# Performance work log

Measured on AMD Instinct MI355X. Metric: run time of the kernel, lower is better.

The kernel has to match this reference:

```python
import jax, jax.numpy as jnp
import numpy as np

TEMPERATURE = 0.07
EPS = 1e-8          # torch cosine_similarity norm clamp
DIAG_FILL = 9e-15   # value masked_fill'ed onto the diagonal BEFORE temperature scaling


def setup_inputs() -> dict:
    key = jax.random.key(0)
    N, D = 16384, 128
    feats = jax.random.normal(key, (N, D), dtype=jnp.float32)
    # unique labels: required for the original torch code's broadcast
    # (-cos_sim[pos_mask] must have exactly N elements)
    labels = jnp.arange(N, dtype=jnp.int32).reshape(N, 1)
    return {"feats": feats, "labels": labels}


def reference(feats, labels):
    # cosine similarity matrix: normalize rows once, then a single GEMM
    norm = jnp.maximum(jnp.linalg.norm(feats, axis=-1, keepdims=True), EPS)
    f = feats / norm
    cos_sim = f @ f.T                                   # [N, N]

    N = cos_sim.shape[0]
    eye = jnp.eye(N, dtype=bool)
    cos_sim = jnp.where(eye, DIAG_FILL, cos_sim)        # masked_fill_(self_mask, 9e-15)
    cos_sim = cos_sim / TEMPERATURE

    pos_mask = labels == labels.T                       # [N, N] bool, one True per row
    # cos_sim[pos_mask] with exactly one positive per row == masked row-sum
    pos = jnp.sum(jnp.where(pos_mask, cos_sim, 0.0), axis=-1)  # [N]

    nll = -pos + jax.nn.logsumexp(cos_sim, axis=-1)     # [N]
    return jnp.mean(nll)
```

## Files before the change

kernel.cpp:

```cpp
#include <hip/hip_runtime.h>
#include <hip/hip_bf16.h>
#include <stdint.h>

typedef __attribute__((ext_vector_type(8))) short short8;
typedef __attribute__((ext_vector_type(4))) float f32x4;

#define N_ROWS 16384
#define DIM 128

constexpr float ALPHA = 4.5398160f;
constexpr float POSC = 1.2857143e-13f;

__device__ __forceinline__ void gload_lds16(const void* g, void* lds) {
  __builtin_amdgcn_global_load_lds(
      (const __attribute__((address_space(1))) void*)(uintptr_t)g,
      (__attribute__((address_space(3))) void*)(uintptr_t)lds,
      16, 0, 0);
}

__global__ void normalize_kernel(const float* __restrict__ feats,
                                 unsigned short* __restrict__ G,
                                 float* __restrict__ rowsum) {
  const int tid  = threadIdx.x;
  const int lane = tid & 63;
  const int row  = blockIdx.x * 4 + (tid >> 6);

  const float2 v = *(const float2*)(feats + (size_t)row * DIM + lane * 2);
  float ss = v.x * v.x + v.y * v.y;
#pragma unroll
  for (int m = 1; m < 64; m <<= 1) ss += __shfl_xor(ss, m);
  const float sc = ALPHA / fmaxf(sqrtf(ss), 1e-8f);

  __hip_bfloat16 h0 = __float2bfloat16(v.x * sc);
  __hip_bfloat16 h1 = __float2bfloat16(v.y * sc);
  unsigned int packed = (unsigned int)(*(unsigned short*)&h0) |
                        ((unsigned int)(*(unsigned short*)&h1) << 16);
  *(unsigned int*)(G + (size_t)row * DIM + lane * 2) = packed;

  if (blockIdx.x < 64) rowsum[blockIdx.x * 256 + tid] = 0.f;
}

__global__ __launch_bounds__(256, 2) void simclr_lse_kernel(
    const unsigned short* __restrict__ G, float* __restrict__ rowsum) {
  const int tid  = threadIdx.x;
  const int lane = tid & 63;
  const int w    = tid >> 6;
  const int wr   = w >> 1;
  const int wc   = w & 1;
  const int c    = lane & 15;
  const int q    = lane >> 4;

  const int p  = blockIdx.x >> 3;
  const int s  = blockIdx.x & 7;
  const int r8 = p & 7;
  const int jb = (s * 129 + r8) >> 3;
  const int je = ((s + 1) * 129 + r8) >> 3;
  const int split = 128 - p;

  __shared__ __align__(16) unsigned short Bbuf[2][128 * 128];

  unsigned goff[8];
#pragma unroll
  for (int t = 0; t < 8; ++t) {
    const int cidx = t * 256 + tid;
    const int col  = cidx >> 4;
    const int kc   = (cidx & 15) ^ (col & 15);
    goff[t] = (unsigned)(col * DIM + kc * 8);
  }

  unsigned boff[4][4];
#pragma unroll
  for (int tc = 0; tc < 4; ++tc)
#pragma unroll
    for (int ks = 0; ks < 4; ++ks) {
      const int col = wc * 64 + tc * 16 + c;
      const int kc  = ks * 4 + q;
      boff[tc][ks] = (unsigned)((col * 16 + (kc ^ c)) * 16);
    }

  const f32x4 zero4 = {0.f, 0.f, 0.f, 0.f};
  const short* Gs = (const short*)G;

  for (int sg = 0; sg < 2; ++sg) {
    int rt, cbeg, nct;
    if (sg == 0) {
      rt   = p;
      cbeg = p + jb;
      nct  = min(je, split) - jb;
    } else {
      rt   = 127 - p;
      const int t0 = max(jb, split);
      cbeg = t0 - 1;
      nct  = je - t0;
    }
    if (nct <= 0) continue;

    const int rbw = rt * 128 + wr * 64;

    short8 afrag[4][4];
#pragma unroll
    for (int tr = 0; tr < 4; ++tr)
#pragma unroll
      for (int ks = 0; ks < 4; ++ks) {
        const int row = rbw + tr * 16 + c;
        afrag[tr][ks] = *(const short8*)(Gs + (size_t)row * DIM + ks * 32 + q * 8);
      }

    float rs[4][4];
#pragma unroll
    for (int tr = 0; tr < 4; ++tr)
#pragma unroll
      for (int r = 0; r < 4; ++r) rs[tr][r] = 0.f;

    {
      const unsigned short* gsrc = G + (size_t)cbeg * 128 * DIM;
#pragma unroll
      for (int t = 0; t < 8; ++t)
        gload_lds16(gsrc + goff[t],
                    (void*)(&Bbuf[0][0] + (size_t)(t * 256 + w * 64) * 8));
    }

    for (int jj = 0; jj < nct; ++jj) {
      const int cur = jj & 1;
      const int ct  = cbeg + jj;
      __syncthreads();

      if (jj + 1 < nct) {
        const unsigned short* gsrc = G + (size_t)(ct + 1) * 128 * DIM;
#pragma unroll
        for (int t = 0; t < 8; ++t)
          gload_lds16(gsrc + goff[t],
                      (void*)(&Bbuf[cur ^ 1][0] + (size_t)(t * 256 + w * 64) * 8));
      }

      const char* bbase = (const char*)&Bbuf[cur][0];
      f32x4 acc[4][4];
#pragma unroll
      for (int ks = 0; ks < 4; ++ks) {
        short8 bfr[4];
#pragma unroll
        for (int tc = 0; tc < 4; ++tc)
          bfr[tc] = *(const short8*)(bbase + boff[tc][ks]);
#pragma unroll
        for (int tr = 0; tr < 4; ++tr)
#pragma unroll
          for (int tc = 0; tc < 4; ++tc) {
            if (ks == 0)
              acc[tr][tc] = __builtin_amdgcn_mfma_f32_16x16x32_bf16(
                  afrag[tr][0], bfr[tc], zero4, 0, 0, 0);
            else
              acc[tr][tc] = __builtin_amdgcn_mfma_f32_16x16x32_bf16(
                  afrag[tr][ks], bfr[tc], acc[tr][tc], 0, 0, 0);
          }
      }

      if (ct == rt && wr == wc) {
#pragma unroll
        for (int tr = 0; tr < 4; ++tr)
#pragma unroll
          for (int r = 0; r < 4; ++r)
            if (c == q * 4 + r) acc[tr][tr][r] = 0.f;
      }

      float cs[4] = {0.f, 0.f, 0.f, 0.f};
#pragma unroll
      for (int tr = 0; tr < 4; ++tr)
#pragma unroll
        for (int tc = 0; tc < 4; ++tc) {
          const float e0 = __builtin_amdgcn_exp2f(acc[tr][tc][0]);
          const float e1 = __builtin_amdgcn_exp2f(acc[tr][tc][1]);
          const float e2 = __builtin_amdgcn_exp2f(acc[tr][tc][2]);
          const float e3 = __builtin_amdgcn_exp2f(acc[tr][tc][3]);
          rs[tr][0] += e0;
          rs[tr][1] += e1;
          rs[tr][2] += e2;
          rs[tr][3] += e3;
          cs[tc] += (e0 + e1) + (e2 + e3);
        }

      if (ct != rt) {
#pragma unroll
        for (int tc = 0; tc < 4; ++tc) {
          float v = cs[tc];
          v += __shfl_xor(v, 16);
          v += __shfl_xor(v, 32);
          if (q == 0)
            atomicAdd(&rowsum[ct * 128 + wc * 64 + tc * 16 + c], v);
        }
      }
    }

#pragma unroll
    for (int tr = 0; tr < 4; ++tr)
#pragma unroll
      for (int r = 0; r < 4; ++r) {
        float v = rs[tr][r];
        v += __shfl_xor(v, 1);
        v += __shfl_xor(v, 2);
        v += __shfl_xor(v, 4);
        v += __shfl_xor(v, 8);
        if (c == 0) atomicAdd(&rowsum[rbw + tr * 16 + q * 4 + r], v);
      }
    __syncthreads();
  }
}

__global__ void finalize_kernel(const float* __restrict__ rowsum,
                                float* __restrict__ out) {
  const int tid = threadIdx.x;
  float local = 0.f;
  for (int i = tid; i < N_ROWS; i += 1024) local += logf(rowsum[i]);
#pragma unroll
  for (int m = 1; m < 64; m <<= 1) local += __shfl_xor(local, m);
  __shared__ float part[16];
  if ((tid & 63) == 0) part[tid >> 6] = local;
  __syncthreads();
  if (tid == 0) {
    float s = 0.f;
#pragma unroll
    for (int i = 0; i < 16; ++i) s += part[i];
    out[0] = s / (float)N_ROWS - POSC;
  }
}

extern "C" void kernel_launch(void* const* d_in, const int* in_sizes, int n_in,
                              void* d_out, int out_size, void* d_ws, size_t ws_size,
                              hipStream_t stream) {
  (void)in_sizes; (void)n_in; (void)out_size; (void)ws_size;
  const float* feats = (const float*)d_in[0];
  unsigned short* G = (unsigned short*)d_ws;
  float* rowsum = (float*)((char*)d_ws + (size_t)N_ROWS * DIM * 2);

  normalize_kernel<<<dim3(N_ROWS / 4), dim3(256), 0, stream>>>(feats, G, rowsum);
  simclr_lse_kernel<<<dim3(512), dim3(256), 0, stream>>>(G, rowsum);
  finalize_kernel<<<dim3(1), dim3(1024), 0, stream>>>(rowsum, d_out ? (float*)d_out : nullptr);
}
```

Before: 116.6 us.

## Replace column atomics with scratch partials and single-buffer LDS tile

Column-sum atomics on mirrored tiles are replaced by plain stores into a per-tile-pair scratch array, and a new column-reduce kernel sums them into rowsum. The LDS double buffer shrinks to one tile buffer loaded synchronously each iteration, which drops the prefetch overlap but halves shared memory, likely to raise occupancy. Column partials are also skipped on diagonal tiles. The cost is an extra kernel launch and a scratch buffer, and global-load latency is now exposed inside the loop.

```diff
diff --git a/kernel.cpp b/kernel.cpp
--- a/kernel.cpp
+++ b/kernel.cpp
@@ -41,7 +41,8 @@
 }
 
 __global__ __launch_bounds__(256, 2) void simclr_lse_kernel(
-    const unsigned short* __restrict__ G, float* __restrict__ rowsum) {
+    const unsigned short* __restrict__ G, float* __restrict__ rowsum,
+    float* __restrict__ scratchC) {
   const int tid  = threadIdx.x;
   const int lane = tid & 63;
   const int w    = tid >> 6;
@@ -57,7 +58,7 @@
   const int je = ((s + 1) * 129 + r8) >> 3;
   const int split = 128 - p;
 
-  __shared__ __align__(16) unsigned short Bbuf[2][128 * 128];
+  __shared__ __align__(16) unsigned short Tbuf[128 * 128];
 
   unsigned goff[8];
 #pragma unroll
@@ -112,35 +113,25 @@
 #pragma unroll
       for (int r = 0; r < 4; ++r) rs[tr][r] = 0.f;
 
-    {
-      const unsigned short* gsrc = G + (size_t)cbeg * 128 * DIM;
-#pragma unroll
-      for (int t = 0; t < 8; ++t)
-        gload_lds16(gsrc + goff[t],
-                    (void*)(&Bbuf[0][0] + (size_t)(t * 256 + w * 64) * 8));
-    }
-
     for (int jj = 0; jj < nct; ++jj) {
-      const int cur = jj & 1;
-      const int ct  = cbeg + jj;
+      const int ct = cbeg + jj;
       __syncthreads();
-
-      if (jj + 1 < nct) {
-        const unsigned short* gsrc = G + (size_t)(ct + 1) * 128 * DIM;
+      {
+        const unsigned short* gsrc = G + (size_t)ct * 128 * DIM;
 #pragma unroll
         for (int t = 0; t < 8; ++t)
           gload_lds16(gsrc + goff[t],
-                      (void*)(&Bbuf[cur ^ 1][0] + (size_t)(t * 256 + w * 64) * 8));
-      }
-
-      const char* bbase = (const char*)&Bbuf[cur][0];
+                      (void*)(Tbuf + (size_t)(t * 256 + w * 64) * 8));
+      }
+      __syncthreads();
+
       f32x4 acc[4][4];
 #pragma unroll
       for (int ks = 0; ks < 4; ++ks) {
         short8 bfr[4];
 #pragma unroll
         for (int tc = 0; tc < 4; ++tc)
-          bfr[tc] = *(const short8*)(bbase + boff[tc][ks]);
+          bfr[tc] = *(const short8*)((const char*)Tbuf + boff[tc][ks]);
 #pragma unroll
         for (int tr = 0; tr < 4; ++tr)
 #pragma unroll
@@ -162,6 +153,7 @@
             if (c == q * 4 + r) acc[tr][tr][r] = 0.f;
       }
 
+      const bool mirror = (ct != rt);
       float cs[4] = {0.f, 0.f, 0.f, 0.f};
 #pragma unroll
       for (int tr = 0; tr < 4; ++tr)
@@ -175,17 +167,17 @@
           rs[tr][1] += e1;
           rs[tr][2] += e2;
           rs[tr][3] += e3;
-          cs[tc] += (e0 + e1) + (e2 + e3);
+          if (mirror) cs[tc] += (e0 + e1) + (e2 + e3);
         }
 
-      if (ct != rt) {
+      if (mirror) {
+        float* slot = scratchC + (size_t)(ct * (ct - 1) / 2 + rt) * 256 + wr * 128;
 #pragma unroll
         for (int tc = 0; tc < 4; ++tc) {
           float v = cs[tc];
           v += __shfl_xor(v, 16);
           v += __shfl_xor(v, 32);
-          if (q == 0)
-            atomicAdd(&rowsum[ct * 128 + wc * 64 + tc * 16 + c], v);
+          if (q == 0) slot[wc * 64 + tc * 16 + c] = v;
         }
       }
     }
@@ -201,8 +193,21 @@
         v += __shfl_xor(v, 8);
         if (c == 0) atomicAdd(&rowsum[rbw + tr * 16 + q * 4 + r], v);
       }
-    __syncthreads();
   }
+}
+
+__global__ void colreduce_kernel(const float* __restrict__ scratchC,
+                                 float* __restrict__ rowsum) {
+  const int ct  = blockIdx.x;
+  const int j   = threadIdx.x & 127;
+  const int h   = threadIdx.x >> 7;
+  __shared__ float tmp[128];
+  float v = 0.f;
+  const float* base = scratchC + (size_t)(ct * (ct - 1) / 2) * 256 + h * 128 + j;
+  for (int rt = 0; rt < ct; ++rt) v += base[(size_t)rt * 256];
+  if (h == 1) tmp[j] = v;
+  __syncthreads();
+  if (h == 0) rowsum[ct * 128 + j] += v + tmp[j];
 }
 
 __global__ void finalize_kernel(const float* __restrict__ rowsum,
@@ -230,8 +235,10 @@
   const float* feats = (const float*)d_in[0];
   unsigned short* G = (unsigned short*)d_ws;
   float* rowsum = (float*)((char*)d_ws + (size_t)N_ROWS * DIM * 2);
+  float* scratchC = rowsum + N_ROWS;
 
   normalize_kernel<<<dim3(N_ROWS / 4), dim3(256), 0, stream>>>(feats, G, rowsum);
-  simclr_lse_kernel<<<dim3(512), dim3(256), 0, stream>>>(G, rowsum);
+  simclr_lse_kernel<<<dim3(512), dim3(256), 0, stream>>>(G, rowsum, scratchC);
+  colreduce_kernel<<<dim3(128), dim3(256), 0, stream>>>(scratchC, rowsum);
   finalize_kernel<<<dim3(1), dim3(1024), 0, stream>>>(rowsum, d_out ? (float*)d_out : nullptr);
 }
```

After: 155.6 us. 33.5% more time.

## Split MFMA tile into two halves, raise wave priority, branchless diagonal mask

Applied to the files above, without the earlier changes.

Splits the per-tile MFMA accumulation into two column halves, loading B fragments just in time. The GEMM section is wrapped in s_setprio so waves in their matrix phase get issue priority over waves doing exp2 work. The diagonal masking becomes a branchless FMA select on the exponentials, and the trailing __syncthreads between the two row segments is dropped. The intent is better overlap of MFMA and transcendental work across the two waves per SIMD, and fewer live accumulators. Removing the barrier risks an LDS race when the second segment's prefetch overwrites a buffer still being read.

```diff
diff --git a/kernel.cpp b/kernel.cpp
--- a/kernel.cpp
+++ b/kernel.cpp
@@ -77,6 +77,10 @@
       const int kc  = ks * 4 + q;
       boff[tc][ks] = (unsigned)((col * 16 + (kc ^ c)) * 16);
     }
+
+  float dsel[4];
+#pragma unroll
+  for (int r = 0; r < 4; ++r) dsel[r] = (c == q * 4 + r) ? 1.f : 0.f;
 
   const f32x4 zero4 = {0.f, 0.f, 0.f, 0.f};
   const short* Gs = (const short*)G;
@@ -134,51 +138,83 @@
       }
 
       const char* bbase = (const char*)&Bbuf[cur][0];
-      f32x4 acc[4][4];
+
+      __builtin_amdgcn_s_setprio(1);
+      f32x4 acc1[4][2];
 #pragma unroll
       for (int ks = 0; ks < 4; ++ks) {
-        short8 bfr[4];
-#pragma unroll
-        for (int tc = 0; tc < 4; ++tc)
-          bfr[tc] = *(const short8*)(bbase + boff[tc][ks]);
-#pragma unroll
-        for (int tr = 0; tr < 4; ++tr)
-#pragma unroll
-          for (int tc = 0; tc < 4; ++tc) {
-            if (ks == 0)
-              acc[tr][tc] = __builtin_amdgcn_mfma_f32_16x16x32_bf16(
-                  afrag[tr][0], bfr[tc], zero4, 0, 0, 0);
-            else
-              acc[tr][tc] = __builtin_amdgcn_mfma_f32_16x16x32_bf16(
-                  afrag[tr][ks], bfr[tc], acc[tr][tc], 0, 0, 0);
-          }
-      }
-
-      if (ct == rt && wr == wc) {
-#pragma unroll
-        for (int tr = 0; tr < 4; ++tr)
-#pragma unroll
-          for (int r = 0; r < 4; ++r)
-            if (c == q * 4 + r) acc[tr][tr][r] = 0.f;
-      }
-
+        const short8 b0 = *(const short8*)(bbase + boff[0][ks]);
+        const short8 b1 = *(const short8*)(bbase + boff[1][ks]);
+#pragma unroll
+        for (int tr = 0; tr < 4; ++tr) {
+          if (ks == 0) {
+            acc1[tr][0] = __builtin_amdgcn_mfma_f32_16x16x32_bf16(
+                afrag[tr][0], b0, zero4, 0, 0, 0);
+            acc1[tr][1] = __builtin_amdgcn_mfma_f32_16x16x32_bf16(
+                afrag[tr][0], b1, zero4, 0, 0, 0);
+          } else {
+            acc1[tr][0] = __builtin_amdgcn_mfma_f32_16x16x32_bf16(
+                afrag[tr][ks], b0, acc1[tr][0], 0, 0, 0);
+            acc1[tr][1] = __builtin_amdgcn_mfma_f32_16x16x32_bf16(
+                afrag[tr][ks], b1, acc1[tr][1], 0, 0, 0);
+          }
+        }
+      }
+      f32x4 acc2[4][2];
+#pragma unroll
+      for (int ks = 0; ks < 4; ++ks) {
+        const short8 b2 = *(const short8*)(bbase + boff[2][ks]);
+        const short8 b3 = *(const short8*)(bbase + boff[3][ks]);
+#pragma unroll
+        for (int tr = 0; tr < 4; ++tr) {
+          if (ks == 0) {
+            acc2[tr][0] = __builtin_amdgcn_mfma_f32_16x16x32_bf16(
+                afrag[tr][0], b2, zero4, 0, 0, 0);
+            acc2[tr][1] = __builtin_amdgcn_mfma_f32_16x16x32_bf16(
+                afrag[tr][0], b3, zero4, 0, 0, 0);
+          } else {
+            acc2[tr][0] = __builtin_amdgcn_mfma_f32_16x16x32_bf16(
+                afrag[tr][ks], b2, acc2[tr][0], 0, 0, 0);
+            acc2[tr][1] = __builtin_amdgcn_mfma_f32_16x16x32_bf16(
+                afrag[tr][ks], b3, acc2[tr][1], 0, 0, 0);
+          }
+        }
+      }
+      __builtin_amdgcn_s_setprio(0);
+
+      const float dj = (ct == rt && wr == wc) ? 1.f : 0.f;
+      float sel[4];
+#pragma unroll
+      for (int r = 0; r < 4; ++r) sel[r] = dj * dsel[r];
+
+      const bool mirror = (ct != rt);
       float cs[4] = {0.f, 0.f, 0.f, 0.f};
 #pragma unroll
       for (int tr = 0; tr < 4; ++tr)
 #pragma unroll
-        for (int tc = 0; tc < 4; ++tc) {
-          const float e0 = __builtin_amdgcn_exp2f(acc[tr][tc][0]);
-          const float e1 = __builtin_amdgcn_exp2f(acc[tr][tc][1]);
-          const float e2 = __builtin_amdgcn_exp2f(acc[tr][tc][2]);
-          const float e3 = __builtin_amdgcn_exp2f(acc[tr][tc][3]);
-          rs[tr][0] += e0;
-          rs[tr][1] += e1;
-          rs[tr][2] += e2;
-          rs[tr][3] += e3;
-          cs[tc] += (e0 + e1) + (e2 + e3);
-        }
-
-      if (ct != rt) {
+        for (int tc = 0; tc < 2; ++tc)
+#pragma unroll
+          for (int r = 0; r < 4; ++r) {
+            float e = __builtin_amdgcn_exp2f(acc1[tr][tc][r]);
+            if (tr == tc) e = fmaf(sel[r], 1.f - e, e);
+            rs[tr][r] += e;
+            cs[tc] += e;
+          }
+#pragma unroll
+      for (int tr = 0; tr < 4; ++tr)
+#pragma unroll
+        for (int tc2 = 0; tc2 < 2; ++tc2) {
+          const int tc = tc2 + 2;
+#pragma unroll
+          for (int r = 0; r < 4; ++r) {
+            float e = __builtin_amdgcn_exp2f(acc2[tr][tc2][r]);
+            if (tr == tc) e = fmaf(sel[r], 1.f - e, e);
+            rs[tr][r] += e;
+            cs[tc] += e;
+          }
+        }
+
+      if (mirror) {
 #pragma unroll
         for (int tc = 0; tc < 4; ++tc) {
           float v = cs[tc];
@@ -201,7 +237,6 @@
         v += __shfl_xor(v, 8);
         if (c == 0) atomicAdd(&rowsum[rbw + tr * 16 + q * 4 + r], v);
       }
-    __syncthreads();
   }
 }
 
```

Result: slower. 120.9 us (+3.7%).

## Split LSE GEMM tiles across eight waves per block with smaller per-wave tiles

Applied to the files above, without the earlier changes.

The block grows from 4 to 8 waves. Each wave now computes a 32x64 sub-tile instead of 64x64, which halves the A fragments, accumulators and row sums held in registers. Global-to-LDS staging is spread over 512 threads, and the diagonal masking is remapped to the new wave layout. The aim is more resident waves to hide MFMA and LDS latency, but each B fragment read from LDS now feeds only half as many MFMAs, so LDS traffic rises. The barrier at the end of each segment is also removed, which risks a race where the next segment's prefetch overwrites a buffer that slower waves are still reading.

```diff
diff --git a/kernel.cpp b/kernel.cpp
--- a/kernel.cpp
+++ b/kernel.cpp
@@ -40,13 +40,13 @@
   if (blockIdx.x < 64) rowsum[blockIdx.x * 256 + tid] = 0.f;
 }
 
-__global__ __launch_bounds__(256, 2) void simclr_lse_kernel(
+__global__ __launch_bounds__(512, 4) void simclr_lse_kernel(
     const unsigned short* __restrict__ G, float* __restrict__ rowsum) {
   const int tid  = threadIdx.x;
   const int lane = tid & 63;
   const int w    = tid >> 6;
-  const int wr   = w >> 1;
-  const int wc   = w & 1;
+  const int wrow = w >> 1;
+  const int wcol = w & 1;
   const int c    = lane & 15;
   const int q    = lane >> 4;
 
@@ -59,24 +59,22 @@
 
   __shared__ __align__(16) unsigned short Bbuf[2][128 * 128];
 
-  unsigned goff[8];
-#pragma unroll
-  for (int t = 0; t < 8; ++t) {
-    const int cidx = t * 256 + tid;
+  unsigned goff[4];
+#pragma unroll
+  for (int t = 0; t < 4; ++t) {
+    const int cidx = t * 512 + tid;
     const int col  = cidx >> 4;
     const int kc   = (cidx & 15) ^ (col & 15);
     goff[t] = (unsigned)(col * DIM + kc * 8);
   }
 
-  unsigned boff[4][4];
-#pragma unroll
-  for (int tc = 0; tc < 4; ++tc)
-#pragma unroll
-    for (int ks = 0; ks < 4; ++ks) {
-      const int col = wc * 64 + tc * 16 + c;
-      const int kc  = ks * 4 + q;
-      boff[tc][ks] = (unsigned)((col * 16 + (kc ^ c)) * 16);
-    }
+  unsigned boff[4];
+#pragma unroll
+  for (int ks = 0; ks < 4; ++ks) {
+    const int col0 = wcol * 64 + c;
+    const int kc   = ks * 4 + q;
+    boff[ks] = (unsigned)((col0 * 16 + (kc ^ c)) * 16);
+  }
 
   const f32x4 zero4 = {0.f, 0.f, 0.f, 0.f};
   const short* Gs = (const short*)G;
@@ -95,29 +93,29 @@
     }
     if (nct <= 0) continue;
 
-    const int rbw = rt * 128 + wr * 64;
-
-    short8 afrag[4][4];
-#pragma unroll
-    for (int tr = 0; tr < 4; ++tr)
+    const int rbw = rt * 128 + wrow * 32;
+
+    short8 afrag[2][4];
+#pragma unroll
+    for (int tr = 0; tr < 2; ++tr)
 #pragma unroll
       for (int ks = 0; ks < 4; ++ks) {
         const int row = rbw + tr * 16 + c;
         afrag[tr][ks] = *(const short8*)(Gs + (size_t)row * DIM + ks * 32 + q * 8);
       }
 
-    float rs[4][4];
-#pragma unroll
-    for (int tr = 0; tr < 4; ++tr)
+    float rs[2][4];
+#pragma unroll
+    for (int tr = 0; tr < 2; ++tr)
 #pragma unroll
       for (int r = 0; r < 4; ++r) rs[tr][r] = 0.f;
 
     {
       const unsigned short* gsrc = G + (size_t)cbeg * 128 * DIM;
 #pragma unroll
-      for (int t = 0; t < 8; ++t)
+      for (int t = 0; t < 4; ++t)
         gload_lds16(gsrc + goff[t],
-                    (void*)(&Bbuf[0][0] + (size_t)(t * 256 + w * 64) * 8));
+                    (void*)(&Bbuf[0][0] + (size_t)(t * 512 + w * 64) * 8));
     }
 
     for (int jj = 0; jj < nct; ++jj) {
@@ -128,21 +126,21 @@
       if (jj + 1 < nct) {
         const unsigned short* gsrc = G + (size_t)(ct + 1) * 128 * DIM;
 #pragma unroll
-        for (int t = 0; t < 8; ++t)
+        for (int t = 0; t < 4; ++t)
           gload_lds16(gsrc + goff[t],
-                      (void*)(&Bbuf[cur ^ 1][0] + (size_t)(t * 256 + w * 64) * 8));
+                      (void*)(&Bbuf[cur ^ 1][0] + (size_t)(t * 512 + w * 64) * 8));
       }
 
       const char* bbase = (const char*)&Bbuf[cur][0];
-      f32x4 acc[4][4];
+      f32x4 acc[2][4];
 #pragma unroll
       for (int ks = 0; ks < 4; ++ks) {
         short8 bfr[4];
 #pragma unroll
         for (int tc = 0; tc < 4; ++tc)
-          bfr[tc] = *(const short8*)(bbase + boff[tc][ks]);
-#pragma unroll
-        for (int tr = 0; tr < 4; ++tr)
+          bfr[tc] = *(const short8*)(bbase + boff[ks] + tc * 4096);
+#pragma unroll
+        for (int tr = 0; tr < 2; ++tr)
 #pragma unroll
           for (int tc = 0; tc < 4; ++tc) {
             if (ks == 0)
@@ -154,17 +152,22 @@
           }
       }
 
-      if (ct == rt && wr == wc) {
-#pragma unroll
-        for (int tr = 0; tr < 4; ++tr)
+      if (ct == rt && (wrow >> 1) == wcol) {
+        if ((wrow & 1) == 0) {
 #pragma unroll
           for (int r = 0; r < 4; ++r)
-            if (c == q * 4 + r) acc[tr][tr][r] = 0.f;
-      }
-
+            if (c == q * 4 + r) { acc[0][0][r] = 0.f; acc[1][1][r] = 0.f; }
+        } else {
+#pragma unroll
+          for (int r = 0; r < 4; ++r)
+            if (c == q * 4 + r) { acc[0][2][r] = 0.f; acc[1][3][r] = 0.f; }
+        }
+      }
+
+      const bool mirror = (ct != rt);
       float cs[4] = {0.f, 0.f, 0.f, 0.f};
 #pragma unroll
-      for (int tr = 0; tr < 4; ++tr)
+      for (int tr = 0; tr < 2; ++tr)
 #pragma unroll
         for (int tc = 0; tc < 4; ++tc) {
           const float e0 = __builtin_amdgcn_exp2f(acc[tr][tc][0]);
@@ -175,23 +178,23 @@
           rs[tr][1] += e1;
           rs[tr][2] += e2;
           rs[tr][3] += e3;
-          cs[tc] += (e0 + e1) + (e2 + e3);
+          if (mirror) cs[tc] += (e0 + e1) + (e2 + e3);
         }
 
-      if (ct != rt) {
+      if (mirror) {
 #pragma unroll
         for (int tc = 0; tc < 4; ++tc) {
           float v = cs[tc];
           v += __shfl_xor(v, 16);
           v += __shfl_xor(v, 32);
           if (q == 0)
-            atomicAdd(&rowsum[ct * 128 + wc * 64 + tc * 16 + c], v);
+            atomicAdd(&rowsum[ct * 128 + wcol * 64 + tc * 16 + c], v);
         }
       }
     }
 
 #pragma unroll
-    for (int tr = 0; tr < 4; ++tr)
+    for (int tr = 0; tr < 2; ++tr)
 #pragma unroll
       for (int r = 0; r < 4; ++r) {
         float v = rs[tr][r];
@@ -201,7 +204,6 @@
         v += __shfl_xor(v, 8);
         if (c == 0) atomicAdd(&rowsum[rbw + tr * 16 + q * 4 + r], v);
       }
-    __syncthreads();
   }
 }
 
@@ -232,6 +234,6 @@
   float* rowsum = (float*)((char*)d_ws + (size_t)N_ROWS * DIM * 2);
 
   normalize_kernel<<<dim3(N_ROWS / 4), dim3(256), 0, stream>>>(feats, G, rowsum);
-  simclr_lse_kernel<<<dim3(512), dim3(256), 0, stream>>>(G, rowsum);
+  simclr_lse_kernel<<<dim3(512), dim3(512), 0, stream>>>(G, rowsum);
   finalize_kernel<<<dim3(1), dim3(1024), 0, stream>>>(rowsum, d_out ? (float*)d_out : nullptr);
 }
```

Result: no change. 116.9 us (+0.3%).
